# Kernel optimization log

Hardware: AMD Instinct MI355X
Metric: run time of the kernel (lower is better)

The kernel has to match this reference:

```python
import jax, jax.numpy as jnp
import numpy as np
from jax.ops import segment_sum

N_NODE, N_EDGE, D_IN, D_HID, N_CLS = 50000, 800000, 64, 64, 40


def setup_inputs() -> dict:
    key = jax.random.key(0)
    k1, k2, k3, k4 = jax.random.split(key, 4)
    x = jax.random.normal(k1, (N_NODE, D_IN), dtype=jnp.float32)
    edge_index = jax.random.randint(k2, (2, N_EDGE), 0, N_NODE, dtype=jnp.int64)
    W1 = jax.random.normal(k3, (D_IN, D_HID), dtype=jnp.float32) * (1.0 / np.sqrt(D_IN))
    b1 = jnp.zeros((D_HID,), dtype=jnp.float32)
    W2 = jax.random.normal(k4, (D_HID, N_CLS), dtype=jnp.float32) * (1.0 / np.sqrt(D_HID))
    b2 = jnp.zeros((N_CLS,), dtype=jnp.float32)
    return {"x": x, "edge_index": edge_index, "W1": W1, "b1": b1, "W2": W2, "b2": b2}


def _att_weights(fea, row, col, n):
    # edge-parallel cosine similarity (sklearn cosine_similarity restricted to edges)
    nrm = jnp.sqrt(jnp.sum(fea * fea, axis=1, keepdims=True))
    fn = fea / jnp.maximum(nrm, 1e-12)
    sim = jnp.sum(fn[row] * fn[col], axis=1)                 # [E]
    sim = jnp.where(sim < 0.1, 0.0, sim)                      # threshold
    # L1 row-normalization (sim >= 0 after threshold)
    rs = segment_sum(sim, row, num_segments=n)                # [N]
    sim_n = jnp.where(sim > 0, sim / jnp.maximum(rs[row], 1e-12), 0.0)
    # degree-based self-loop weight lam = 1/(deg+1)
    deg = segment_sum((sim > 0).astype(fea.dtype), row, num_segments=n)
    lam = 1.0 / (deg + 1.0)
    # exp applied only to stored (nonzero) entries; zeroed edges stay 0
    w_edge = jnp.where(sim > 0, jnp.exp(sim_n), 0.0)          # [E]
    w_self = jnp.exp(lam)                                     # [N] self-loop weights
    return w_edge, w_self


def _gcn(h, W, b, row, col, w_edge, w_self, n):
    # symmetric-norm GCN over weighted edges + explicit self loops
    deg = segment_sum(w_edge, row, num_segments=n) + w_self
    dinv = 1.0 / jnp.sqrt(jnp.maximum(deg, 1e-12))
    h = h @ W                                                 # [N, F]
    coef = w_edge * dinv[row] * dinv[col]                     # [E]
    out = segment_sum(coef[:, None] * h[col], row, num_segments=n)
    out = out + (w_self * dinv * dinv)[:, None] * h + b
    return out


def reference(x, edge_index, W1, b1, W2, b2):
    n = x.shape[0]
    row, col = edge_index[0], edge_index[1]
    # layer 1: attention coefs from raw features
    w1e, w1s = _att_weights(x, row, col, n)
    h = jax.nn.relu(_gcn(x, W1, b1, row, col, w1e, w1s, n))
    # layer 2: attention coefs recomputed on hidden features (dropout = eval mode)
    w2e, w2s = _att_weights(h, row, col, n)
    out = _gcn(h, W2, b2, row, col, w2e, w2s, n)
    return jax.nn.log_softmax(out, axis=1)
```

## Files before the change

### kernel.cpp

```cpp
#include <hip/hip_runtime.h>
#include <math.h>


#define ATT_CAP 96
#define EPB     2048
#define RPB     128
#define NBUCK_MAX 512
#define CAPB    4096

typedef _Float16 half4 __attribute__((ext_vector_type(4)));

__global__ void k_normfn(const float* __restrict__ fea, float* __restrict__ fn, int n)
{
    int gid  = blockIdx.x * blockDim.x + threadIdx.x;
    int wid  = gid >> 6;
    int lane = threadIdx.x & 63;
    if (wid >= n) return;
    float v = fea[(size_t)wid * 64 + lane];
    float s = v * v;
#pragma unroll
    for (int off = 32; off > 0; off >>= 1) s += __shfl_xor(s, off);
    float inv = 1.0f / fmaxf(sqrtf(s), 1e-12f);
    fn[(size_t)wid * 64 + lane] = v * inv;
}

__global__ void k_bhist(const int* __restrict__ row, int* __restrict__ btot,
                        int E, int nbuck)
{
    __shared__ int lh[NBUCK_MAX];
    int b = blockIdx.x;
    int ebeg = b * EPB, eend = ebeg + EPB; if (eend > E) eend = E;
    for (int i = threadIdx.x; i < nbuck; i += blockDim.x) lh[i] = 0;
    __syncthreads();
    for (int e = ebeg + threadIdx.x; e < eend; e += blockDim.x)
        atomicAdd(&lh[row[e] >> 7], 1);
    __syncthreads();
    for (int i = threadIdx.x; i < nbuck; i += blockDim.x)
        if (lh[i]) atomicAdd(btot + i, lh[i]);
}

__global__ void k_bscan(const int* __restrict__ btot, int* __restrict__ bbase,
                        int* __restrict__ gcur, int nbuck)
{
    int lane = threadIdx.x;
    int K = (nbuck + 63) / 64;
    int beg = lane * K;
    int s = 0;
    for (int i = 0; i < K; ++i) { int idx = beg + i; if (idx < nbuck) s += btot[idx]; }
    int incl = s;
#pragma unroll
    for (int off = 1; off < 64; off <<= 1) {
        int v = __shfl_up(incl, off);
        if (lane >= off) incl += v;
    }
    int run = incl - s;
    for (int i = 0; i < K; ++i) {
        int idx = beg + i;
        if (idx < nbuck) { bbase[idx] = run; gcur[idx] = run; run += btot[idx]; }
    }
    if (lane == 63) bbase[nbuck] = incl;
}

__global__ void k_bscat(const int* __restrict__ row, const int* __restrict__ col,
                        int* __restrict__ gcur, int* __restrict__ ebuf, int E, int nbuck)
{
    __shared__ int lh[NBUCK_MAX];
    __shared__ int lbase[NBUCK_MAX];
    int b = blockIdx.x;
    int ebeg = b * EPB, eend = ebeg + EPB; if (eend > E) eend = E;
    int rr[8], cc[8];
    int ne = 0;
    for (int i = threadIdx.x; i < nbuck; i += blockDim.x) lh[i] = 0;
    __syncthreads();
    for (int e = ebeg + threadIdx.x; e < eend; e += blockDim.x) {
        int r = row[e], c = col[e];
        rr[ne] = r; cc[ne] = c; ++ne;
        atomicAdd(&lh[r >> 7], 1);
    }
    __syncthreads();
    for (int i = threadIdx.x; i < nbuck; i += blockDim.x) {
        int cnt = lh[i];
        if (cnt) lbase[i] = atomicAdd(gcur + i, cnt);
        lh[i] = 0;
    }
    __syncthreads();
    for (int k = 0; k < ne; ++k) {
        int j = rr[k] >> 7;
        int pos = lbase[j] + atomicAdd(&lh[j], 1);
        ebuf[pos] = ((rr[k] & (RPB - 1)) << 16) | cc[k];
    }
}

__global__ void k_csr(const int* __restrict__ ebuf, const int* __restrict__ bbase,
                      int* __restrict__ rptr, int* __restrict__ col_s, int N, int E)
{
    __shared__ int pk[CAPB];
    __shared__ int lcol[CAPB];
    __shared__ int lcnt[RPB], lexc[RPB], lcur[RPB];
    int j = blockIdx.x;
    int beg = bbase[j], end = bbase[j + 1];
    int m = end - beg; if (m > CAPB) m = CAPB;
    int tid = threadIdx.x;
    for (int i = tid; i < m; i += blockDim.x) pk[i] = ebuf[beg + i];
    if (tid < RPB) lcnt[tid] = 0;
    __syncthreads();
    for (int i = tid; i < m; i += blockDim.x) atomicAdd(&lcnt[pk[i] >> 16], 1);
    __syncthreads();
    if (tid < 64) {
        int a = lcnt[2 * tid], b2 = lcnt[2 * tid + 1];
        int s = a + b2;
        int incl = s;
#pragma unroll
        for (int off = 1; off < 64; off <<= 1) {
            int v = __shfl_up(incl, off);
            if (tid >= off) incl += v;
        }
        int base = incl - s;
        lexc[2 * tid] = base;     lexc[2 * tid + 1] = base + a;
        lcur[2 * tid] = base;     lcur[2 * tid + 1] = base + a;
    }
    __syncthreads();
    for (int i = tid; i < m; i += blockDim.x) {
        int v = pk[i];
        int p = atomicAdd(&lcur[v >> 16], 1);
        lcol[p] = v & 0xFFFF;
    }
    __syncthreads();
    for (int i = tid; i < m; i += blockDim.x) col_s[beg + i] = lcol[i];
    if (tid < RPB) {
        int r = j * RPB + tid;
        if (r < N) rptr[r] = beg + lexc[tid];
    }
    if (j == 0 && tid == 0) rptr[N] = E;
}

__global__ void k_att(const float* __restrict__ fn,
                      const int* __restrict__ rptr, const int* __restrict__ col_s,
                      int2* __restrict__ cw, int* __restrict__ lend,
                      float* __restrict__ dinv, float* __restrict__ selfc, int n)
{
    __shared__ float ssim[4][ATT_CAP];
    __shared__ int   scol[4][ATT_CAP];
    int wib  = threadIdx.x >> 6;
    int wid  = blockIdx.x * 4 + wib;
    int lane = threadIdx.x & 63;
    if (wid >= n) return;
    int sub = lane & 7;
    int grp = lane >> 3;
    int beg = rptr[wid], end = rptr[wid + 1];
    int deg_all = end - beg;

    const float4* frp = (const float4*)(fn + (size_t)wid * 64);
    float4 a0 = frp[sub * 2], a1 = frp[sub * 2 + 1];

    float rs_part = 0.0f;
    int ngrp = (deg_all + 7) >> 3;
    for (int g = 0; g < ngrp; ++g) {
        int li = g * 8 + grp;
        float s = 0.0f; int c = 0;
        bool valid = (li < deg_all);
        if (valid) {
            c = col_s[beg + li];
            const float4* fcp = (const float4*)(fn + (size_t)c * 64);
            float4 b0 = fcp[sub * 2], b1 = fcp[sub * 2 + 1];
            float p = a0.x * b0.x + a0.y * b0.y + a0.z * b0.z + a0.w * b0.w
                    + a1.x * b1.x + a1.y * b1.y + a1.z * b1.z + a1.w * b1.w;
            p += __shfl_xor(p, 1);
            p += __shfl_xor(p, 2);
            p += __shfl_xor(p, 4);
            s = (p < 0.1f) ? 0.0f : p;
        }
        if (sub == 0 && valid) {
            if (li < ATT_CAP) { ssim[wib][li] = s; scol[wib][li] = c; }
            if (s > 0.0f) rs_part += s;
        }
    }
#pragma unroll
    for (int off = 32; off > 0; off >>= 1) rs_part += __shfl_xor(rs_part, off);
    float denom = fmaxf(rs_part, 1e-12f);

    int   nlive = 0;
    float sw_lane = 0.0f;
    for (int base = 0; base < deg_all; base += 64) {
        int li = base + lane;
        bool valid = (li < deg_all);
        float s = 0.0f; int c = 0;
        if (valid) {
            if (li < ATT_CAP) { s = ssim[wib][li]; c = scol[wib][li]; }
            else {
                c = col_s[beg + li];
                const float* fr = fn + (size_t)wid * 64;
                const float* fc = fn + (size_t)c * 64;
                float p = 0.0f;
                for (int k = 0; k < 64; ++k) p += fr[k] * fc[k];
                s = (p < 0.1f) ? 0.0f : p;
            }
        }
        float w = (valid && s > 0.0f) ? expf(s / denom) : 0.0f;
        unsigned long long M = __ballot(w > 0.0f);
        int rank = __popcll(M & ((1ull << lane) - 1ull));
        if (w > 0.0f) {
            int2 pw; pw.x = c; pw.y = __float_as_int(w);
            cw[beg + nlive + rank] = pw;
            sw_lane += w;
        }
        nlive += __popcll(M);
    }
#pragma unroll
    for (int off = 32; off > 0; off >>= 1) sw_lane += __shfl_xor(sw_lane, off);

    if (lane == 0) {
        float wself = expf(1.0f / ((float)nlive + 1.0f));
        float D  = sw_lane + wself;
        float di = rsqrtf(fmaxf(D, 1e-12f));
        lend[wid]  = beg + nlive;
        dinv[wid]  = di;
        selfc[wid] = wself * di;
    }
}

template <int F, typename InT, typename OutT>
__global__ void k_gemm(const InT* __restrict__ fea, const float* __restrict__ W,
                       const float* __restrict__ scale, OutT* __restrict__ out, int n)
{
    constexpr int R = 256 / F;
    __shared__ float sW[64 * F];
    __shared__ float sX[R * 64];
    int tid = threadIdx.x;
    for (int i = tid; i < 64 * F; i += 256) sW[i] = W[i];
    int base = blockIdx.x * R;
    for (int i = tid; i < R * 64; i += 256) {
        int rr = base + i / 64;
        sX[i] = (rr < n) ? (float)fea[(size_t)rr * 64 + (i & 63)] : 0.0f;
    }
    __syncthreads();
    int rl = tid / F, j = tid % F;
    if (rl >= R) return;
    int r = base + rl;
    if (r >= n) return;
    float acc = 0.0f;
#pragma unroll
    for (int k = 0; k < 64; ++k) acc = fmaf(sX[rl * 64 + k], sW[k * F + j], acc);
    out[(size_t)r * F + j] = (OutT)(acc * scale[r]);
}

template <int F, typename Vec4>
__device__ inline float agg_core_t(const Vec4* __restrict__ hdv,
                                   const int2* __restrict__ cw,
                                   int beg, int lend_, int lane)
{
    int q  = lane & 15;
    int eg = lane >> 4;
    bool qact = (F == 64) ? true : (q < (F >> 2));
    float acc0 = 0.f, acc1 = 0.f, acc2 = 0.f, acc3 = 0.f;
    for (int base = beg; base < lend_; base += 64) {
        int idx = base + lane;
        int cv = 0; float wv = 0.0f;
        if (idx < lend_) { int2 pw = cw[idx]; cv = pw.x; wv = __int_as_float(pw.y); }
        int cnt = lend_ - base; if (cnt > 64) cnt = 64;
        for (int j = 0; j < cnt; j += 4) {
            int   c = __shfl(cv, j + eg);
            float w = __shfl(wv, j + eg);
            if (qact) {
                Vec4 hv = hdv[(size_t)c * (F >> 2) + q];
                acc0 += w * (float)hv.x;
                acc1 += w * (float)hv.y;
                acc2 += w * (float)hv.z;
                acc3 += w * (float)hv.w;
            }
        }
    }
    acc0 += __shfl_xor(acc0, 16); acc0 += __shfl_xor(acc0, 32);
    acc1 += __shfl_xor(acc1, 16); acc1 += __shfl_xor(acc1, 32);
    acc2 += __shfl_xor(acc2, 16); acc2 += __shfl_xor(acc2, 32);
    acc3 += __shfl_xor(acc3, 16); acc3 += __shfl_xor(acc3, 32);
    int srcq = lane >> 2;
    float a0 = __shfl(acc0, srcq);
    float a1 = __shfl(acc1, srcq);
    float a2 = __shfl(acc2, srcq);
    float a3 = __shfl(acc3, srcq);
    int k = lane & 3;
    return (k == 0) ? a0 : (k == 1) ? a1 : (k == 2) ? a2 : a3;
}

__global__ void k_agg64(const float* __restrict__ hd, const int2* __restrict__ cw,
                        const float* __restrict__ dinv, const float* __restrict__ selfc,
                        const float* __restrict__ b, const int* __restrict__ row_ptr,
                        const int* __restrict__ lend,
                        _Float16* __restrict__ hrelu16, float* __restrict__ fnh, int n)
{
    int gid  = blockIdx.x * blockDim.x + threadIdx.x;
    int wid  = gid >> 6;
    int lane = threadIdx.x & 63;
    if (wid >= n) return;
    int beg = row_ptr[wid], le = lend[wid];
    float accf = agg_core_t<64>((const float4*)hd, cw, beg, le, lane);
    float hs  = hd[(size_t)wid * 64 + lane];
    float v = dinv[wid] * accf + selfc[wid] * hs + b[lane];
    v = fmaxf(v, 0.0f);
    hrelu16[(size_t)wid * 64 + lane] = (_Float16)v;
    float s = v * v;
#pragma unroll
    for (int off = 32; off > 0; off >>= 1) s += __shfl_xor(s, off);
    float inv = 1.0f / fmaxf(sqrtf(s), 1e-12f);
    fnh[(size_t)wid * 64 + lane] = v * inv;
}

__global__ void k_agg40_lsm(const _Float16* __restrict__ hd2, const int2* __restrict__ cw,
                            const float* __restrict__ dinv, const float* __restrict__ selfc,
                            const float* __restrict__ b, const int* __restrict__ row_ptr,
                            const int* __restrict__ lend,
                            float* __restrict__ out, int n)
{
    constexpr int F = 40;
    int gid  = blockIdx.x * blockDim.x + threadIdx.x;
    int wid  = gid >> 6;
    int lane = threadIdx.x & 63;
    if (wid >= n) return;
    int beg = row_ptr[wid], le = lend[wid];
    float accf = agg_core_t<F>((const half4*)hd2, cw, beg, le, lane);
    bool active = (lane < F);
    float v = 0.0f;
    if (active) {
        float hs = (float)hd2[(size_t)wid * F + lane];
        v = dinv[wid] * accf + selfc[wid] * hs + b[lane];
    }
    float m = active ? v : -__builtin_inff();
#pragma unroll
    for (int off = 32; off > 0; off >>= 1) m = fmaxf(m, __shfl_xor(m, off));
    float ex = active ? expf(v - m) : 0.0f;
    float s = ex;
#pragma unroll
    for (int off = 32; off > 0; off >>= 1) s += __shfl_xor(s, off);
    if (active) out[(size_t)wid * F + lane] = v - m - logf(s);
}

extern "C" void kernel_launch(void* const* d_in, const int* in_sizes, int n_in,
                              void* d_out, int out_size, void* d_ws, size_t ws_size,
                              hipStream_t stream)
{
    const float* x  = (const float*)d_in[0];
    const int*   ei = (const int*)d_in[1];
    const float* W1 = (const float*)d_in[2];
    const float* b1 = (const float*)d_in[3];
    const float* W2 = (const float*)d_in[4];
    const float* b2 = (const float*)d_in[5];
    float* out = (float*)d_out;

    const int N = in_sizes[0] / 64;
    const int E = in_sizes[1] / 2;
    const int* row = ei;
    const int* col = ei + E;

    const int nblkA = (E + EPB - 1) / EPB;
    const int nbuck = (N + RPB - 1) / RPB;

    char* p = (char*)d_ws;
    auto alloc = [&](size_t bytes) -> char* {
        char* r = p; p += (bytes + 255) & ~(size_t)255; return r;
    };
    float*     fn     = (float*)alloc((size_t)N * 64 * 4);
    float*     dinv   = (float*)alloc((size_t)N * 4);
    float*     selfc  = (float*)alloc((size_t)N * 4);
    float*     hd1    = (float*)alloc((size_t)N * 64 * 4);
    _Float16*  hrelu  = (_Float16*)alloc((size_t)N * 64 * 2);
    _Float16*  hd2    = (_Float16*)alloc((size_t)N * 40 * 2);
    float*     fnh    = (float*)alloc((size_t)N * 64 * 4);
    int*       rptr   = (int*)alloc((size_t)(N + 1) * 4);
    int*       lendv  = (int*)alloc((size_t)N * 4);
    int*       col_s  = (int*)alloc((size_t)E * 4);
    int2*      cw     = (int2*)alloc((size_t)E * 8);
    int*       ebuf   = (int*)alloc((size_t)E * 4);
    int*       btot   = (int*)alloc((size_t)nbuck * 4);
    int*       bbase  = (int*)alloc((size_t)(nbuck + 1) * 4);
    int*       gcur   = (int*)alloc((size_t)nbuck * 4);

    const int TB = 256;
    int blk_nodeWave = (N * 64 + TB - 1) / TB;
    int blk_node4    = (N + 3) / 4;

    hipMemsetAsync(btot, 0, (size_t)nbuck * 4, stream);

    k_bhist<<<nblkA, TB, 0, stream>>>(row, btot, E, nbuck);
    k_bscan<<<1, 64, 0, stream>>>(btot, bbase, gcur, nbuck);
    k_bscat<<<nblkA, TB, 0, stream>>>(row, col, gcur, ebuf, E, nbuck);
    k_csr<<<nbuck, TB, 0, stream>>>(ebuf, bbase, rptr, col_s, N, E);

    k_normfn<<<blk_nodeWave, TB, 0, stream>>>(x, fn, N);
    k_att<<<blk_node4, TB, 0, stream>>>(fn, rptr, col_s, cw, lendv, dinv, selfc, N);
    k_gemm<64, float, float><<<(N + 3) / 4, TB, 0, stream>>>(x, W1, dinv, hd1, N);
    k_agg64<<<blk_nodeWave, TB, 0, stream>>>(hd1, cw, dinv, selfc, b1,
                                             rptr, lendv, hrelu, fnh, N);

    k_att<<<blk_node4, TB, 0, stream>>>(fnh, rptr, col_s, cw, lendv, dinv, selfc, N);
    k_gemm<40, _Float16, _Float16><<<(N + 5) / 6, TB, 0, stream>>>(hrelu, W2, dinv, hd2, N);
    k_agg40_lsm<<<blk_nodeWave, TB, 0, stream>>>(hd2, cw, dinv, selfc, b2,
                                                 rptr, lendv, out, N);
}
```

Measured before the change: 286.8 us.

## Drop histogram and scan passes by scattering into fixed-capacity bucket slots

```diff
diff --git a/kernel.cpp b/kernel.cpp
--- a/kernel.cpp
+++ b/kernel.cpp
@@ -22,43 +22,6 @@
     for (int off = 32; off > 0; off >>= 1) s += __shfl_xor(s, off);
     float inv = 1.0f / fmaxf(sqrtf(s), 1e-12f);
     fn[(size_t)wid * 64 + lane] = v * inv;
-}
-
-__global__ void k_bhist(const int* __restrict__ row, int* __restrict__ btot,
-                        int E, int nbuck)
-{
-    __shared__ int lh[NBUCK_MAX];
-    int b = blockIdx.x;
-    int ebeg = b * EPB, eend = ebeg + EPB; if (eend > E) eend = E;
-    for (int i = threadIdx.x; i < nbuck; i += blockDim.x) lh[i] = 0;
-    __syncthreads();
-    for (int e = ebeg + threadIdx.x; e < eend; e += blockDim.x)
-        atomicAdd(&lh[row[e] >> 7], 1);
-    __syncthreads();
-    for (int i = threadIdx.x; i < nbuck; i += blockDim.x)
-        if (lh[i]) atomicAdd(btot + i, lh[i]);
-}
-
-__global__ void k_bscan(const int* __restrict__ btot, int* __restrict__ bbase,
-                        int* __restrict__ gcur, int nbuck)
-{
-    int lane = threadIdx.x;
-    int K = (nbuck + 63) / 64;
-    int beg = lane * K;
-    int s = 0;
-    for (int i = 0; i < K; ++i) { int idx = beg + i; if (idx < nbuck) s += btot[idx]; }
-    int incl = s;
-#pragma unroll
-    for (int off = 1; off < 64; off <<= 1) {
-        int v = __shfl_up(incl, off);
-        if (lane >= off) incl += v;
-    }
-    int run = incl - s;
-    for (int i = 0; i < K; ++i) {
-        int idx = beg + i;
-        if (idx < nbuck) { bbase[idx] = run; gcur[idx] = run; run += btot[idx]; }
-    }
-    if (lane == 63) bbase[nbuck] = incl;
 }
 
 __global__ void k_bscat(const int* __restrict__ row, const int* __restrict__ col,
@@ -80,7 +43,7 @@
     __syncthreads();
     for (int i = threadIdx.x; i < nbuck; i += blockDim.x) {
         int cnt = lh[i];
-        if (cnt) lbase[i] = atomicAdd(gcur + i, cnt);
+        if (cnt) lbase[i] = i * CAPB + atomicAdd(gcur + i, cnt);
         lh[i] = 0;
     }
     __syncthreads();
@@ -91,18 +54,30 @@
     }
 }
 
-__global__ void k_csr(const int* __restrict__ ebuf, const int* __restrict__ bbase,
-                      int* __restrict__ rptr, int* __restrict__ col_s, int N, int E)
+__global__ void k_csr(const int* __restrict__ ebuf, const int* __restrict__ gcur,
+                      int* __restrict__ rptr, int* __restrict__ col_s,
+                      int N, int E, int nbuck)
 {
     __shared__ int pk[CAPB];
     __shared__ int lcol[CAPB];
     __shared__ int lcnt[RPB], lexc[RPB], lcur[RPB];
+    __shared__ int spart[4];
     int j = blockIdx.x;
-    int beg = bbase[j], end = bbase[j + 1];
-    int m = end - beg; if (m > CAPB) m = CAPB;
     int tid = threadIdx.x;
-    for (int i = tid; i < m; i += blockDim.x) pk[i] = ebuf[beg + i];
+    int lane = tid & 63, wave = tid >> 6;
+
+    int part = 0;
+    for (int i = tid; i < j; i += blockDim.x) part += gcur[i];
+#pragma unroll
+    for (int off = 32; off > 0; off >>= 1) part += __shfl_xor(part, off);
+    if (lane == 0) spart[wave] = part;
     if (tid < RPB) lcnt[tid] = 0;
+    __syncthreads();
+    int beg = spart[0] + spart[1] + spart[2] + spart[3];
+    int m = gcur[j]; if (m > CAPB) m = CAPB;
+
+    const int* seg = ebuf + (size_t)j * CAPB;
+    for (int i = tid; i < m; i += blockDim.x) pk[i] = seg[i];
     __syncthreads();
     for (int i = tid; i < m; i += blockDim.x) atomicAdd(&lcnt[pk[i] >> 16], 1);
     __syncthreads();
@@ -370,21 +345,17 @@
     int*       lendv  = (int*)alloc((size_t)N * 4);
     int*       col_s  = (int*)alloc((size_t)E * 4);
     int2*      cw     = (int2*)alloc((size_t)E * 8);
-    int*       ebuf   = (int*)alloc((size_t)E * 4);
-    int*       btot   = (int*)alloc((size_t)nbuck * 4);
-    int*       bbase  = (int*)alloc((size_t)(nbuck + 1) * 4);
+    int*       ebuf   = (int*)alloc((size_t)nbuck * CAPB * 4);
     int*       gcur   = (int*)alloc((size_t)nbuck * 4);
 
     const int TB = 256;
     int blk_nodeWave = (N * 64 + TB - 1) / TB;
     int blk_node4    = (N + 3) / 4;
 
-    hipMemsetAsync(btot, 0, (size_t)nbuck * 4, stream);
-
-    k_bhist<<<nblkA, TB, 0, stream>>>(row, btot, E, nbuck);
-    k_bscan<<<1, 64, 0, stream>>>(btot, bbase, gcur, nbuck);
+    hipMemsetAsync(gcur, 0, (size_t)nbuck * 4, stream);
+
     k_bscat<<<nblkA, TB, 0, stream>>>(row, col, gcur, ebuf, E, nbuck);
-    k_csr<<<nbuck, TB, 0, stream>>>(ebuf, bbase, rptr, col_s, N, E);
+    k_csr<<<nbuck, TB, 0, stream>>>(ebuf, gcur, rptr, col_s, N, E, nbuck);
 
     k_normfn<<<blk_nodeWave, TB, 0, stream>>>(x, fn, N);
     k_att<<<blk_node4, TB, 0, stream>>>(fn, rptr, col_s, cw, lendv, dinv, selfc, N);
```

Result: faster. 273.8 us (-4.5%).
